# Optimization experiments

Measured on AMD Instinct MI355X. Metric: run time of the kernel, lower is better.

The kernel has to match this reference:

```python
import jax, jax.numpy as jnp
import numpy as np

EPS = 1e-08
SPARSITY = 0.1  # fraction of (node, hyperedge) incidences set to 1


def setup_inputs() -> dict:
    key = jax.random.key(0)
    k_x, k_w, k_h, k_W, k_b = jax.random.split(key, 5)
    B, N, E, Din, Dout = 8, 4096, 2048, 256, 256
    x = jax.random.normal(k_x, (B, N, Din), dtype=jnp.float32)
    edge_weight = jax.random.uniform(k_w, (E,), dtype=jnp.float32)
    H = (jax.random.uniform(k_h, (N, E)) < SPARSITY).astype(jnp.float32)
    # nn.Linear params
    bound = 1.0 / np.sqrt(Din)
    W = jax.random.uniform(k_W, (Dout, Din), minval=-bound, maxval=bound, dtype=jnp.float32)
    b = jax.random.uniform(k_b, (Dout,), minval=-bound, maxval=bound, dtype=jnp.float32)
    return {"x": x, "edge_weight": edge_weight, "H": H, "W": W, "b": b}


def _build_adjacency(H, edge_weight):
    # dv = H @ diag(w) @ 1 = H @ w ; de = H.sum(0)
    dv = H @ edge_weight                      # [N]
    de = H.sum(axis=0)                        # [E]
    dv_is = jnp.power(dv + EPS, -0.5)         # Dv^{-1/2} diagonal
    de_inv = jnp.power(de + EPS, -1.0)        # De^{-1} diagonal
    # A = Dv^{-1/2} H W De^{-1} H^T Dv^{-1/2}; apply diagonals as row/col scales
    Hw = H * (edge_weight * de_inv)[None, :]  # [N, E]
    A = (dv_is[:, None] * (Hw @ H.T)) * dv_is[None, :]  # [N, N]
    return A


def reference(x, edge_weight, H, W, b):
    A = _build_adjacency(H, edge_weight)
    xw = jnp.einsum('bnd,od->bno', x, W) + b  # Linear: [B, N, Dout]
    out = jnp.einsum('ij,bjd->bid', A, xw)    # hypergraph propagation
    return out
```

## Files before the change

### kernel.cpp

```cpp
#include <hip/hip_runtime.h>
#include <hip/hip_bf16.h>

typedef __hip_bfloat16 bf16;
typedef __bf16 bfx8 __attribute__((ext_vector_type(8)));
typedef float f32x4 __attribute__((ext_vector_type(4)));

#define BM 128

typedef __attribute__((address_space(3))) void lds_void_t;
typedef const __attribute__((address_space(1))) void gbl_void_t;

__global__ void prep_kernel(const float* __restrict__ H, const float* __restrict__ w,
                            bf16* __restrict__ HT, bf16* __restrict__ Hb,
                            float* __restrict__ de, float* __restrict__ dvr, int N, int E) {
    __shared__ bf16 tile[64][65];
    __shared__ float cred[4][64];
    __shared__ float rred[4][64];
    int eb = blockIdx.x * 64, nb = blockIdx.y * 64;
    int tid = threadIdx.x;
    int c = tid & 63, g = tid >> 6;

    float cs = 0.f;
#pragma unroll
    for (int k = 0; k < 16; k++) {
        int r = g + (k << 2);
        float v = H[(size_t)(nb + r) * E + eb + c];
        bf16 bv = __float2bfloat16(v);
        tile[r][c] = bv;
        Hb[(size_t)(nb + r) * E + eb + c] = bv;
        cs += v;
    }
    cred[g][c] = cs;
    __syncthreads();
    if (g == 0) {
        float s = cred[0][c] + cred[1][c] + cred[2][c] + cred[3][c];
        atomicAdd(&de[eb + c], s);
    }
    float rs = 0.f;
#pragma unroll
    for (int k = 0; k < 16; k++) {
        int cc = g + (k << 2);
        rs += __bfloat162float(tile[c][cc]) * w[eb + cc];
    }
    rred[g][c] = rs;
    __syncthreads();
    if (g == 1) {
        float s = rred[0][c] + rred[1][c] + rred[2][c] + rred[3][c];
        atomicAdd(&dvr[nb + c], s);
    }
#pragma unroll
    for (int k = 0; k < 16; k++) {
        int r = g + (k << 2);
        HT[(size_t)(eb + r) * N + nb + c] = tile[c][r];
    }
}

__global__ void finalize_kernel(const float* __restrict__ dvr, const float* __restrict__ de,
                                const float* __restrict__ w, float* __restrict__ dv_is,
                                float* __restrict__ wsc, int N, int E) {
    int i = blockIdx.x * 256 + threadIdx.x;
    if (i < N) dv_is[i] = rsqrtf(dvr[i] + 1e-8f);
    if (i < E) wsc[i] = w[i] / (de[i] + 1e-8f);
}

__global__ void combine_kernel(const bf16* __restrict__ s0, const bf16* __restrict__ s1,
                               const float* __restrict__ wsc, bf16* __restrict__ tt) {
    size_t i = ((size_t)blockIdx.x * 256 + threadIdx.x) * 8;
    size_t e = i & 2047;
    bfx8 a = *(const bfx8*)&s0[i];
    bfx8 b = *(const bfx8*)&s1[i];
    bfx8 v;
#pragma unroll
    for (int t = 0; t < 8; t++)
        v[t] = (__bf16)(((float)a[t] + (float)b[t]) * wsc[e + t]);
    *(bfx8*)&tt[i] = v;
}

template <int MODE, int RY>
__global__ __launch_bounds__(256) void gemm_bt_async(
    const bf16* __restrict__ A, const bf16* __restrict__ Bt, int Kst, int kLen,
    void* __restrict__ Cv, int ldc,
    const float* __restrict__ rvec, const float* __restrict__ cvec) {
    __shared__ __align__(16) bf16 SA[2][BM * 32];
    __shared__ __align__(16) bf16 SB[2][64 * 32];

    const int lin = blockIdx.y * gridDim.x + blockIdx.x;
    const int xcd = lin & 7, sidx = lin >> 3;
    const int bx = (xcd & 3) * 8 + (sidx & 7);
    const int by = (xcd >> 2) * RY + (sidx >> 3);

    const int kBase = (MODE == 3) ? blockIdx.z * kLen : 0;

    const int tid     = threadIdx.x;
    const int rowBase = by * BM;
    const int colBase = bx * 64;
    const int wave = tid >> 6, lane = tid & 63;
    const int wr = (wave >> 1) * 64;
    const int wc = (wave & 1) * 32;
    const int lcol = lane & 15, quad = lane >> 4;

    const int sr = tid >> 2, skc = (tid & 3) << 3;
    const bf16* a0 = &A[(size_t)(rowBase + sr) * Kst + kBase + skc];
    const bf16* a1 = a0 + (size_t)64 * Kst;
    const bf16* b0 = &Bt[(size_t)(colBase + sr) * Kst + kBase + skc];
    bf16* d_a0[2] = {&SA[0][sr * 32 + skc], &SA[1][sr * 32 + skc]};
    bf16* d_a1[2] = {&SA[0][(sr + 64) * 32 + skc], &SA[1][(sr + 64) * 32 + skc]};
    bf16* d_b0[2] = {&SB[0][sr * 32 + skc], &SB[1][sr * 32 + skc]};

    f32x4 acc[4][2];
#pragma unroll
    for (int i = 0; i < 4; i++)
#pragma unroll
        for (int j = 0; j < 2; j++) acc[i][j] = (f32x4){0.f, 0.f, 0.f, 0.f};

    for (int k0 = 0; k0 < kLen; k0 += 64) {
#pragma unroll
        for (int h = 0; h < 2; h++) {
            int kk = k0 + h * 32;
            __builtin_amdgcn_global_load_lds((gbl_void_t*)(a0 + kk), (lds_void_t*)d_a0[h], 16, 0, 0);
            __builtin_amdgcn_global_load_lds((gbl_void_t*)(a1 + kk), (lds_void_t*)d_a1[h], 16, 0, 0);
            __builtin_amdgcn_global_load_lds((gbl_void_t*)(b0 + kk), (lds_void_t*)d_b0[h], 16, 0, 0);
        }
        __syncthreads();

#pragma unroll
        for (int h = 0; h < 2; h++) {
            bfx8 af[4], bfr[2];
#pragma unroll
            for (int i = 0; i < 4; i++)
                af[i] = *(const bfx8*)&SA[h][(wr + i * 16 + lcol) * 32 + quad * 8];
#pragma unroll
            for (int j = 0; j < 2; j++)
                bfr[j] = *(const bfx8*)&SB[h][(wc + j * 16 + lcol) * 32 + quad * 8];
#pragma unroll
            for (int i = 0; i < 4; i++)
#pragma unroll
                for (int j = 0; j < 2; j++)
                    acc[i][j] = __builtin_amdgcn_mfma_f32_16x16x32_bf16(af[i], bfr[j], acc[i][j], 0, 0, 0);
        }
        __syncthreads();
    }

    bf16*  Cb = (bf16*)Cv;
    float* Cf = (float*)Cv;
    const size_t sliceOff = (MODE == 3) ? (size_t)blockIdx.z * 4194304 : 0;
#pragma unroll
    for (int i = 0; i < 4; i++) {
#pragma unroll
        for (int j = 0; j < 2; j++) {
#pragma unroll
            for (int r = 0; r < 4; r++) {
                int grow = rowBase + wr + i * 16 + quad * 4 + r;
                int gcol = colBase + wc + j * 16 + lcol;
                float v = acc[i][j][r];
                if (MODE == 3) {
                    Cb[sliceOff + (size_t)grow * ldc + gcol] = __float2bfloat16(v);
                } else {
                    Cf[(size_t)(gcol >> 8) * 1048576 + (size_t)grow * 256 + (gcol & 255)] =
                        v * rvec[grow];
                }
            }
        }
    }
}

__global__ __launch_bounds__(256) void gemm_bt_conv(
    const float* __restrict__ A, const float* __restrict__ B, int K,
    bf16* __restrict__ C, int ldc,
    const float* __restrict__ rvec, const float* __restrict__ cvec,
    long long bStride, long long cStride) {
    __shared__ __align__(16) bf16 As[BM * 40];
    __shared__ __align__(16) bf16 Bs[BM * 40];

    const float* Bp = B + (size_t)blockIdx.z * (size_t)bStride;
    bf16*        Cp = C + (size_t)blockIdx.z * (size_t)cStride;

    const int tid     = threadIdx.x;
    const int rowBase = blockIdx.y * BM;
    const int colBase = blockIdx.x * BM;
    const int wave = tid >> 6, lane = tid & 63;
    const int wr = (wave >> 1) * 64;
    const int wc = (wave & 1) * 64;
    const int lcol = lane & 15, quad = lane >> 4;

    f32x4 acc[4][4];
#pragma unroll
    for (int i = 0; i < 4; i++)
#pragma unroll
        for (int j = 0; j < 4; j++) acc[i][j] = (f32x4){0.f, 0.f, 0.f, 0.f};

    for (int k0 = 0; k0 < K; k0 += 32) {
#pragma unroll
        for (int c = 0; c < 2; c++) {
            int ch = tid + c * 256;
            int r = ch >> 2, kc = (ch & 3) << 3;
            size_t aoff = (size_t)(rowBase + r) * K + k0 + kc;
            size_t boff = (size_t)(colBase + r) * K + k0 + kc;
            f32x4 p0 = *(const f32x4*)&A[aoff];
            f32x4 p1 = *(const f32x4*)&A[aoff + 4];
            bfx8 va;
#pragma unroll
            for (int t = 0; t < 4; t++) { va[t] = (__bf16)p0[t]; va[4 + t] = (__bf16)p1[t]; }
            *(bfx8*)&As[r * 40 + kc] = va;
            f32x4 q0 = *(const f32x4*)&Bp[boff];
            f32x4 q1 = *(const f32x4*)&Bp[boff + 4];
            bfx8 vb;
#pragma unroll
            for (int t = 0; t < 4; t++) { vb[t] = (__bf16)q0[t]; vb[4 + t] = (__bf16)q1[t]; }
            *(bfx8*)&Bs[r * 40 + kc] = vb;
        }
        __syncthreads();

        bfx8 af[4], bfr[4];
#pragma unroll
        for (int i = 0; i < 4; i++)
            af[i] = *(const bfx8*)&As[(wr + i * 16 + lcol) * 40 + quad * 8];
#pragma unroll
        for (int j = 0; j < 4; j++)
            bfr[j] = *(const bfx8*)&Bs[(wc + j * 16 + lcol) * 40 + quad * 8];
#pragma unroll
        for (int i = 0; i < 4; i++)
#pragma unroll
            for (int j = 0; j < 4; j++)
                acc[i][j] = __builtin_amdgcn_mfma_f32_16x16x32_bf16(af[i], bfr[j], acc[i][j], 0, 0, 0);
        __syncthreads();
    }

#pragma unroll
    for (int i = 0; i < 4; i++) {
#pragma unroll
        for (int j = 0; j < 4; j++) {
#pragma unroll
            for (int r = 0; r < 4; r++) {
                int grow = rowBase + wr + i * 16 + quad * 4 + r;
                int gcol = colBase + wc + j * 16 + lcol;
                float v = (acc[i][j][r] + rvec[grow]) * cvec[gcol];
                Cp[(size_t)grow * ldc + gcol] = __float2bfloat16(v);
            }
        }
    }
}

extern "C" void kernel_launch(void* const* d_in, const int* in_sizes, int n_in,
                              void* d_out, int out_size, void* d_ws, size_t ws_size,
                              hipStream_t stream) {
    const float* x    = (const float*)d_in[0];
    const float* ew   = (const float*)d_in[1];
    const float* H    = (const float*)d_in[2];
    const float* W    = (const float*)d_in[3];
    const float* bias = (const float*)d_in[4];
    float* out = (float*)d_out;

    const int N = 4096, E = 2048;

    char* ws = (char*)d_ws;
    float* de    = (float*)(ws);
    float* dvr   = (float*)(ws + 8192);
    float* dv_is = (float*)(ws + 24576);
    float* wsc   = (float*)(ws + 40960);
    bf16*  HT    = (bf16*)(ws + 65536);
    bf16*  xs_t  = (bf16*)(ws + 65536 + 16777216);
    bf16*  t_t   = (bf16*)(ws + 65536 + 2 * 16777216);

    bf16* Hb     = (bf16*)d_out;
    bf16* slices = (bf16*)((char*)d_out + 16777216);

    hipMemsetAsync(ws, 0, 24576, stream);

    prep_kernel<<<dim3(E / 64, N / 64), 256, 0, stream>>>(H, ew, HT, Hb, de, dvr, N, E);
    finalize_kernel<<<dim3(16), 256, 0, stream>>>(dvr, de, ew, dv_is, wsc, N, E);

    gemm_bt_conv<<<dim3(4096 / BM, 256 / BM, 8), 256, 0, stream>>>(
        W, x, 256, xs_t, 4096, bias, dv_is, 1048576LL, 1048576LL);

    gemm_bt_async<3, 8><<<dim3(32, 16, 2), 256, 0, stream>>>(
        xs_t, HT, 4096, 2048, slices, 2048, nullptr, nullptr);

    combine_kernel<<<dim3(2048), 256, 0, stream>>>(
        slices, slices + 4194304, wsc, t_t);

    hipMemcpyAsync(xs_t, Hb, 16777216, hipMemcpyDeviceToDevice, stream);

    gemm_bt_async<2, 16><<<dim3(32, 32), 256, 0, stream>>>(
        (const bf16*)xs_t, t_t, 2048, 2048, out, 0, dv_is, nullptr);
}
```

Measured before the change: 234.3 us.

## Replace GEMMs with 256x256-tile 8-wave pipelined kernel and split-K reductions

Both big GEMMs now run on a new 512-thread kernel with 256x256 output tiles, swizzled LDS staging through global_load_lds, double-buffered k-tiles interleaved with MFMA phases at raised priority, and split-K into bf16 slices. The first GEMM uses 4-way split-K with a 4-input combine. The second uses 2-way split-K plus a combine kernel that applies the Dv^-1/2 scale and writes fp32 output. The bf16 copy of H is now produced by a transpose kernel from HT instead of a second write in prep plus a device memcpy. This trades extra slice traffic and launches for far higher per-tile reuse and deeper pipelining.

```diff
diff --git a/kernel.cpp b/kernel.cpp
--- a/kernel.cpp
+++ b/kernel.cpp
@@ -11,7 +11,7 @@
 typedef const __attribute__((address_space(1))) void gbl_void_t;
 
 __global__ void prep_kernel(const float* __restrict__ H, const float* __restrict__ w,
-                            bf16* __restrict__ HT, bf16* __restrict__ Hb,
+                            bf16* __restrict__ HT,
                             float* __restrict__ de, float* __restrict__ dvr, int N, int E) {
     __shared__ bf16 tile[64][65];
     __shared__ float cred[4][64];
@@ -27,7 +27,6 @@
         float v = H[(size_t)(nb + r) * E + eb + c];
         bf16 bv = __float2bfloat16(v);
         tile[r][c] = bv;
-        Hb[(size_t)(nb + r) * E + eb + c] = bv;
         cs += v;
     }
     cred[g][c] = cs;
@@ -61,107 +60,6 @@
     int i = blockIdx.x * 256 + threadIdx.x;
     if (i < N) dv_is[i] = rsqrtf(dvr[i] + 1e-8f);
     if (i < E) wsc[i] = w[i] / (de[i] + 1e-8f);
-}
-
-__global__ void combine_kernel(const bf16* __restrict__ s0, const bf16* __restrict__ s1,
-                               const float* __restrict__ wsc, bf16* __restrict__ tt) {
-    size_t i = ((size_t)blockIdx.x * 256 + threadIdx.x) * 8;
-    size_t e = i & 2047;
-    bfx8 a = *(const bfx8*)&s0[i];
-    bfx8 b = *(const bfx8*)&s1[i];
-    bfx8 v;
-#pragma unroll
-    for (int t = 0; t < 8; t++)
-        v[t] = (__bf16)(((float)a[t] + (float)b[t]) * wsc[e + t]);
-    *(bfx8*)&tt[i] = v;
-}
-
-template <int MODE, int RY>
-__global__ __launch_bounds__(256) void gemm_bt_async(
-    const bf16* __restrict__ A, const bf16* __restrict__ Bt, int Kst, int kLen,
-    void* __restrict__ Cv, int ldc,
-    const float* __restrict__ rvec, const float* __restrict__ cvec) {
-    __shared__ __align__(16) bf16 SA[2][BM * 32];
-    __shared__ __align__(16) bf16 SB[2][64 * 32];
-
-    const int lin = blockIdx.y * gridDim.x + blockIdx.x;
-    const int xcd = lin & 7, sidx = lin >> 3;
-    const int bx = (xcd & 3) * 8 + (sidx & 7);
-    const int by = (xcd >> 2) * RY + (sidx >> 3);
-
-    const int kBase = (MODE == 3) ? blockIdx.z * kLen : 0;
-
-    const int tid     = threadIdx.x;
-    const int rowBase = by * BM;
-    const int colBase = bx * 64;
-    const int wave = tid >> 6, lane = tid & 63;
-    const int wr = (wave >> 1) * 64;
-    const int wc = (wave & 1) * 32;
-    const int lcol = lane & 15, quad = lane >> 4;
-
-    const int sr = tid >> 2, skc = (tid & 3) << 3;
-    const bf16* a0 = &A[(size_t)(rowBase + sr) * Kst + kBase + skc];
-    const bf16* a1 = a0 + (size_t)64 * Kst;
-    const bf16* b0 = &Bt[(size_t)(colBase + sr) * Kst + kBase + skc];
-    bf16* d_a0[2] = {&SA[0][sr * 32 + skc], &SA[1][sr * 32 + skc]};
-    bf16* d_a1[2] = {&SA[0][(sr + 64) * 32 + skc], &SA[1][(sr + 64) * 32 + skc]};
-    bf16* d_b0[2] = {&SB[0][sr * 32 + skc], &SB[1][sr * 32 + skc]};
-
-    f32x4 acc[4][2];
-#pragma unroll
-    for (int i = 0; i < 4; i++)
-#pragma unroll
-        for (int j = 0; j < 2; j++) acc[i][j] = (f32x4){0.f, 0.f, 0.f, 0.f};
-
-    for (int k0 = 0; k0 < kLen; k0 += 64) {
-#pragma unroll
-        for (int h = 0; h < 2; h++) {
-            int kk = k0 + h * 32;
-            __builtin_amdgcn_global_load_lds((gbl_void_t*)(a0 + kk), (lds_void_t*)d_a0[h], 16, 0, 0);
-            __builtin_amdgcn_global_load_lds((gbl_void_t*)(a1 + kk), (lds_void_t*)d_a1[h], 16, 0, 0);
-            __builtin_amdgcn_global_load_lds((gbl_void_t*)(b0 + kk), (lds_void_t*)d_b0[h], 16, 0, 0);
-        }
-        __syncthreads();
-
-#pragma unroll
-        for (int h = 0; h < 2; h++) {
-            bfx8 af[4], bfr[2];
-#pragma unroll
-            for (int i = 0; i < 4; i++)
-                af[i] = *(const bfx8*)&SA[h][(wr + i * 16 + lcol) * 32 + quad * 8];
-#pragma unroll
-            for (int j = 0; j < 2; j++)
-                bfr[j] = *(const bfx8*)&SB[h][(wc + j * 16 + lcol) * 32 + quad * 8];
-#pragma unroll
-            for (int i = 0; i < 4; i++)
-#pragma unroll
-                for (int j = 0; j < 2; j++)
-                    acc[i][j] = __builtin_amdgcn_mfma_f32_16x16x32_bf16(af[i], bfr[j], acc[i][j], 0, 0, 0);
-        }
-        __syncthreads();
-    }
-
-    bf16*  Cb = (bf16*)Cv;
-    float* Cf = (float*)Cv;
-    const size_t sliceOff = (MODE == 3) ? (size_t)blockIdx.z * 4194304 : 0;
-#pragma unroll
-    for (int i = 0; i < 4; i++) {
-#pragma unroll
-        for (int j = 0; j < 2; j++) {
-#pragma unroll
-            for (int r = 0; r < 4; r++) {
-                int grow = rowBase + wr + i * 16 + quad * 4 + r;
-                int gcol = colBase + wc + j * 16 + lcol;
-                float v = acc[i][j][r];
-                if (MODE == 3) {
-                    Cb[sliceOff + (size_t)grow * ldc + gcol] = __float2bfloat16(v);
-                } else {
-                    Cf[(size_t)(gcol >> 8) * 1048576 + (size_t)grow * 256 + (gcol & 255)] =
-                        v * rvec[grow];
-                }
-            }
-        }
-    }
 }
 
 __global__ __launch_bounds__(256) void gemm_bt_conv(
@@ -241,6 +139,219 @@
     }
 }
 
+
+#define STG_A(cb, h, u) do { \
+    __builtin_amdgcn_global_load_lds((gbl_void_t*)(ga##h##0 + (size_t)(u) * 64), \
+        (lds_void_t*)&SM[(cb) * 16384 + (h) * 8192 + dOff], 16, 0, 0); \
+    __builtin_amdgcn_global_load_lds((gbl_void_t*)(ga##h##1 + (size_t)(u) * 64), \
+        (lds_void_t*)&SM[(cb) * 16384 + (h) * 8192 + 4096 + dOff], 16, 0, 0); \
+} while (0)
+
+#define STG_B(cb, h, u) do { \
+    __builtin_amdgcn_global_load_lds((gbl_void_t*)(gb##h##0 + (size_t)(u) * 64), \
+        (lds_void_t*)&SM[32768 + (cb) * 16384 + (h) * 8192 + dOff], 16, 0, 0); \
+    __builtin_amdgcn_global_load_lds((gbl_void_t*)(gb##h##1 + (size_t)(u) * 64), \
+        (lds_void_t*)&SM[32768 + (cb) * 16384 + (h) * 8192 + 4096 + dOff], 16, 0, 0); \
+} while (0)
+
+#define LDA_(cb, qi, i, kk) \
+    (*(const bfx8*)&SM[(cb) * 16384 + aBase + ((qi) * 64 + (i) * 16) * 64 + ra##kk])
+#define LDB_(cb, j, kk) \
+    (*(const bfx8*)&SM[32768 + (cb) * 16384 + bjb[j] + ra##kk])
+
+#define PH_MFMA(I0, J0) do { \
+    __builtin_amdgcn_s_setprio(1); \
+    _Pragma("unroll") \
+    for (int i_ = 0; i_ < 4; i_++) { \
+        _Pragma("unroll") \
+        for (int jj_ = 0; jj_ < 2; jj_++) { \
+            acc[(I0) + i_][(J0) + jj_] = __builtin_amdgcn_mfma_f32_16x16x32_bf16( \
+                af[i_][0], bf[(J0) + jj_][0], acc[(I0) + i_][(J0) + jj_], 0, 0, 0); \
+            acc[(I0) + i_][(J0) + jj_] = __builtin_amdgcn_mfma_f32_16x16x32_bf16( \
+                af[i_][1], bf[(J0) + jj_][1], acc[(I0) + i_][(J0) + jj_], 0, 0, 0); \
+        } \
+    } \
+    __builtin_amdgcn_s_setprio(0); \
+} while (0)
+
+#define KTILE(cb, uA, uB) do { \
+     \
+    _Pragma("unroll") \
+    for (int i_ = 0; i_ < 4; i_++) { af[i_][0] = LDA_(cb, 0, i_, 0); af[i_][1] = LDA_(cb, 0, i_, 1); } \
+    _Pragma("unroll") \
+    for (int j_ = 0; j_ < 2; j_++) { bf[j_][0] = LDB_(cb, j_, 0); bf[j_][1] = LDB_(cb, j_, 1); } \
+    STG_A((cb) ^ 1, 0, uA); \
+    __builtin_amdgcn_s_barrier(); \
+    PH_MFMA(0, 0); \
+    __builtin_amdgcn_s_barrier(); \
+     \
+    _Pragma("unroll") \
+    for (int j_ = 0; j_ < 2; j_++) { bf[2 + j_][0] = LDB_(cb, 2 + j_, 0); bf[2 + j_][1] = LDB_(cb, 2 + j_, 1); } \
+    STG_A((cb) ^ 1, 1, uA); \
+    __builtin_amdgcn_s_barrier(); \
+    PH_MFMA(0, 2); \
+    __builtin_amdgcn_s_barrier(); \
+     \
+    _Pragma("unroll") \
+    for (int i_ = 0; i_ < 4; i_++) { af[i_][0] = LDA_(cb, 1, i_, 0); af[i_][1] = LDA_(cb, 1, i_, 1); } \
+    STG_B(cb, 0, uB); \
+    __builtin_amdgcn_s_barrier(); \
+    PH_MFMA(4, 2); \
+    __builtin_amdgcn_s_barrier(); \
+     \
+    STG_B(cb, 1, uB); \
+    __builtin_amdgcn_s_barrier(); \
+    PH_MFMA(4, 0); \
+    asm volatile("s_waitcnt vmcnt(4)" ::: "memory"); \
+    __builtin_amdgcn_s_barrier(); \
+} while (0)
+
+__global__ __launch_bounds__(512, 2) void gemm8ph(
+    const bf16* __restrict__ A, const bf16* __restrict__ Bt, int Kst, int kLen,
+    bf16* __restrict__ S0, bf16* __restrict__ S1, bf16* __restrict__ S2, bf16* __restrict__ S3,
+    int ldc) {
+    __shared__ __align__(16) bf16 SM[65536];
+
+    const int nx = gridDim.x, ny = gridDim.y;
+    const int nwg = nx * ny * gridDim.z;
+    const int lin = (blockIdx.z * ny + blockIdx.y) * nx + blockIdx.x;
+    const int cpx = nwg >> 3;
+    const int swz = (lin & 7) * cpx + (lin >> 3);
+    const int bx = swz % nx;
+    const int t1 = swz / nx;
+    const int by = t1 % ny;
+    const int bz = t1 / ny;
+    bf16* Cs = (bz == 0) ? S0 : (bz == 1) ? S1 : (bz == 2) ? S2 : S3;
+    const int kBase = bz * kLen;
+    const int NT = kLen >> 6;
+
+    const int tid = threadIdx.x;
+    const int lane = tid & 63, wave = tid >> 6;
+    const int lcol = lane & 15, quad = lane >> 4;
+    const int wr = (wave >> 2) * 128, wc = (wave & 3) * 64;
+    const int aBase = (wave >> 2) * 8192;
+    const int xr = lcol & 7;
+
+    const int rowBase = by * 256, colBase = bx * 256;
+
+    const int ra0 = lcol * 64 + ((quad ^ xr) << 3);
+    const int ra1 = lcol * 64 + (((4 + quad) ^ xr) << 3);
+    int bjb[4];
+#pragma unroll
+    for (int j = 0; j < 4; j++) {
+        int rg = wc + j * 16;
+        bjb[j] = ((rg >> 7) * 8192) + ((rg & 127) * 64);
+    }
+
+    const int srow = tid >> 3, slot = tid & 7;
+    const int r0 = srow, r1 = srow + 64;
+    const int sx0 = (slot ^ (r0 & 7)) << 3;
+    const int sx1 = (slot ^ (r1 & 7)) << 3;
+    const bf16* ga00 = A + (size_t)(rowBase + r0) * Kst + kBase + sx0;
+    const bf16* ga01 = A + (size_t)(rowBase + r1) * Kst + kBase + sx1;
+    const bf16* ga10 = A + (size_t)(rowBase + 128 + r0) * Kst + kBase + sx0;
+    const bf16* ga11 = A + (size_t)(rowBase + 128 + r1) * Kst + kBase + sx1;
+    const bf16* gb00 = Bt + (size_t)(colBase + r0) * Kst + kBase + sx0;
+    const bf16* gb01 = Bt + (size_t)(colBase + r1) * Kst + kBase + sx1;
+    const bf16* gb10 = Bt + (size_t)(colBase + 128 + r0) * Kst + kBase + sx0;
+    const bf16* gb11 = Bt + (size_t)(colBase + 128 + r1) * Kst + kBase + sx1;
+    const int dOff = tid * 8;
+
+    f32x4 acc[8][4];
+#pragma unroll
+    for (int i = 0; i < 8; i++)
+#pragma unroll
+        for (int j = 0; j < 4; j++) acc[i][j] = (f32x4){0.f, 0.f, 0.f, 0.f};
+    bfx8 af[4][2], bf[4][2];
+
+    STG_A(0, 0, 0); STG_A(0, 1, 0); STG_B(0, 0, 0); STG_B(0, 1, 0);
+    STG_B(1, 0, 1); STG_B(1, 1, 1);
+    asm volatile("s_waitcnt vmcnt(4)" ::: "memory");
+    __builtin_amdgcn_s_barrier();
+
+    const int nPairs = NT >> 1;
+    for (int it = 0; it < nPairs; ++it) {
+        int u1 = 2 * it + 1;
+        int u2 = 2 * it + 2; if (u2 > NT - 1) u2 = NT - 1;
+        int u3 = 2 * it + 3; if (u3 > NT - 1) u3 = NT - 1;
+        KTILE(0, u1, u2);
+        KTILE(1, u2, u3);
+    }
+
+#pragma unroll
+    for (int i = 0; i < 8; i++) {
+#pragma unroll
+        for (int j = 0; j < 4; j++) {
+#pragma unroll
+            for (int r = 0; r < 4; r++) {
+                int grow = rowBase + wr + i * 16 + quad * 4 + r;
+                int gcol = colBase + wc + j * 16 + lcol;
+                Cs[(size_t)grow * ldc + gcol] = __float2bfloat16(acc[i][j][r]);
+            }
+        }
+    }
+}
+
+__global__ void combine4_kernel(const bf16* __restrict__ s0, const bf16* __restrict__ s1,
+                                const bf16* __restrict__ s2, const bf16* __restrict__ s3,
+                                const float* __restrict__ wsc, bf16* __restrict__ tt) {
+    size_t i = ((size_t)blockIdx.x * 256 + threadIdx.x) * 8;
+    int e = (int)(i & 2047);
+    bfx8 a = *(const bfx8*)&s0[i];
+    bfx8 b = *(const bfx8*)&s1[i];
+    bfx8 c = *(const bfx8*)&s2[i];
+    bfx8 d = *(const bfx8*)&s3[i];
+    bfx8 v;
+#pragma unroll
+    for (int t = 0; t < 8; t++)
+        v[t] = (__bf16)((((float)a[t] + (float)b[t]) + ((float)c[t] + (float)d[t])) * wsc[e + t]);
+    *(bfx8*)&tt[i] = v;
+}
+
+__global__ void transpose_kernel(const bf16* __restrict__ src, bf16* __restrict__ dst,
+                                 int R, int C) {
+    __shared__ __bf16 t[64][68];
+    int cb = blockIdx.x * 64, rb = blockIdx.y * 64;
+    int tid = threadIdx.x;
+    int lc = tid & 7, lr = tid >> 3;
+#pragma unroll
+    for (int p = 0; p < 2; p++) {
+        int r = lr + p * 32;
+        bfx8 v = *(const bfx8*)&src[(size_t)(rb + r) * C + cb + lc * 8];
+#pragma unroll
+        for (int q = 0; q < 8; q++) t[r][lc * 8 + q] = v[q];
+    }
+    __syncthreads();
+#pragma unroll
+    for (int p = 0; p < 2; p++) {
+        int c = lr + p * 32;
+        bfx8 v;
+#pragma unroll
+        for (int q = 0; q < 8; q++) v[q] = t[lc * 8 + q][c];
+        *(bfx8*)&dst[(size_t)(cb + c) * R + rb + lc * 8] = v;
+    }
+}
+
+__global__ void combine_out_kernel(const bf16* __restrict__ sA, const bf16* __restrict__ sB,
+                                   const float* __restrict__ dv_is, float* __restrict__ out) {
+    size_t t8 = ((size_t)blockIdx.x * 256 + threadIdx.x) * 8;
+    int o = (int)(t8 & 255);
+    int n = (int)((t8 >> 8) & 4095);
+    int b = (int)(t8 >> 20);
+    size_t si = (size_t)n * 2048 + b * 256 + o;
+    bfx8 a = *(const bfx8*)&sA[si];
+    bfx8 bb = *(const bfx8*)&sB[si];
+    float d = dv_is[n];
+    f32x4 v0, v1;
+#pragma unroll
+    for (int t = 0; t < 4; t++) {
+        v0[t] = d * ((float)a[t] + (float)bb[t]);
+        v1[t] = d * ((float)a[4 + t] + (float)bb[4 + t]);
+    }
+    *(f32x4*)&out[t8] = v0;
+    *(f32x4*)&out[t8 + 4] = v1;
+}
+
 extern "C" void kernel_launch(void* const* d_in, const int* in_sizes, int n_in,
                               void* d_out, int out_size, void* d_ws, size_t ws_size,
                               hipStream_t stream) {
@@ -249,7 +360,6 @@
     const float* H    = (const float*)d_in[2];
     const float* W    = (const float*)d_in[3];
     const float* bias = (const float*)d_in[4];
-    float* out = (float*)d_out;
 
     const int N = 4096, E = 2048;
 
@@ -260,27 +370,31 @@
     float* wsc   = (float*)(ws + 40960);
     bf16*  HT    = (bf16*)(ws + 65536);
     bf16*  xs_t  = (bf16*)(ws + 65536 + 16777216);
-    bf16*  t_t   = (bf16*)(ws + 65536 + 2 * 16777216);
-
-    bf16* Hb     = (bf16*)d_out;
-    bf16* slices = (bf16*)((char*)d_out + 16777216);
-
-    hipMemsetAsync(ws, 0, 24576, stream);
-
-    prep_kernel<<<dim3(E / 64, N / 64), 256, 0, stream>>>(H, ew, HT, Hb, de, dvr, N, E);
+    bf16*  t_t   = (bf16*)(ws + 65536 + 33554432);
+
+    bf16* s0 = (bf16*)d_out;
+    bf16* s1 = s0 + 4194304;
+    bf16* s2 = s0 + 2 * 4194304;
+    bf16* s3 = s0 + 3 * 4194304;
+    bf16* Hb = (bf16*)d_out;
+    bf16* k5a = HT;
+    bf16* k5b = xs_t;
+
+    (void)hipMemsetAsync(ws, 0, 24576, stream);
+
+    prep_kernel<<<dim3(E / 64, N / 64), 256, 0, stream>>>(H, ew, HT, de, dvr, N, E);
     finalize_kernel<<<dim3(16), 256, 0, stream>>>(dvr, de, ew, dv_is, wsc, N, E);
 
     gemm_bt_conv<<<dim3(4096 / BM, 256 / BM, 8), 256, 0, stream>>>(
         W, x, 256, xs_t, 4096, bias, dv_is, 1048576LL, 1048576LL);
 
-    gemm_bt_async<3, 8><<<dim3(32, 16, 2), 256, 0, stream>>>(
-        xs_t, HT, 4096, 2048, slices, 2048, nullptr, nullptr);
-
-    combine_kernel<<<dim3(2048), 256, 0, stream>>>(
-        slices, slices + 4194304, wsc, t_t);
-
-    hipMemcpyAsync(xs_t, Hb, 16777216, hipMemcpyDeviceToDevice, stream);
-
-    gemm_bt_async<2, 16><<<dim3(32, 32), 256, 0, stream>>>(
-        (const bf16*)xs_t, t_t, 2048, 2048, out, 0, dv_is, nullptr);
-}
+    gemm8ph<<<dim3(8, 8, 4), 512, 0, stream>>>(xs_t, HT, 4096, 1024, s0, s1, s2, s3, 2048);
+
+    combine4_kernel<<<dim3(2048), 256, 0, stream>>>(s0, s1, s2, s3, wsc, t_t);
+
+    transpose_kernel<<<dim3(64, 32), 256, 0, stream>>>(HT, Hb, 2048, 4096);
+
+    gemm8ph<<<dim3(8, 16, 2), 512, 0, stream>>>(Hb, t_t, 2048, 1024, k5a, k5b, k5a, k5a, 2048);
+
+    combine_out_kernel<<<dim3(4096), 256, 0, stream>>>(k5a, k5b, dv_is, (float*)d_out);
+}
```

Measured after the change: 216.1 us. 1.08x faster.
